# Performance work log

Measured on AMD Instinct MI355X. Metric: run time of the kernel, lower is better.

## Reference

```python
import jax, jax.numpy as jnp
import numpy as np

MODES = 2
N = 6000
KNN = 15
NODES = 512
LC = 3  # number of hidden layers
SCALE = 0.05


def _gen_coo(n, knn):
    # One (row, col) pair per CK_inputs entry: node i couples to 2*(knn+1)
    # neighbors i-knn .. i+knn+1, clipped to valid range. Duplicates at the
    # boundaries are summed on scatter (matches torch sparse coalesce()).
    offsets = np.arange(-knn, knn + 2)            # 2*(knn+1) offsets
    rows = np.repeat(np.arange(n), 2 * (knn + 1))
    cols = np.clip((np.arange(n)[:, None] + offsets[None, :]).reshape(-1), 0, n - 1)
    return rows.astype(np.int32), cols.astype(np.int32)


def setup_inputs() -> dict:
    key = jax.random.key(0)
    k0, k1, k2, k3 = jax.random.split(key, 4)
    CK_inputs = jax.random.normal(k0, (N, 2 * (KNN + 1), 3), dtype=jnp.float32)
    W_in = (jax.random.normal(k1, (3, NODES), dtype=jnp.float32) * SCALE)
    b_in = jnp.zeros((NODES,), dtype=jnp.float32)
    Wh = (jax.random.normal(k2, (LC, NODES, NODES), dtype=jnp.float32) * SCALE)
    bh = jnp.zeros((LC, NODES), dtype=jnp.float32)
    W_out = (jax.random.normal(k3, (NODES, MODES ** 2), dtype=jnp.float32) * SCALE)
    b_out = jnp.zeros((MODES ** 2,), dtype=jnp.float32)
    rows_np, cols_np = _gen_coo(N, KNN)
    return {
        "CK_inputs": CK_inputs,
        "W_in": W_in, "b_in": b_in,
        "Wh": Wh, "bh": bh,
        "W_out": W_out, "b_out": b_out,
        "rows": jnp.asarray(rows_np), "cols": jnp.asarray(cols_np),
    }


def reference(CK_inputs, W_in, b_in, Wh, bh, W_out, b_out, rows, cols):
    n = CK_inputs.shape[0]
    modes = int(np.sqrt(b_out.shape[0]))
    # MLP over all E = N*2*(Knn+1) couplings: [E,3] -> [E, modes^2]
    x = CK_inputs.reshape(-1, 3)
    h = jax.nn.relu(x @ W_in + b_in)
    for l in range(Wh.shape[0]):  # small fixed layer count
        h = jax.nn.relu(h @ Wh[l] + bh[l])
    vals = (h @ W_out + b_out).reshape(-1, modes, modes)  # [E, mi, mj]
    # Fused scatter-add: original builds modes^2 sparse COO tensors with
    # indices (r*modes+mi, c*modes+mj), sums, coalesces, densifies. That is
    # exactly dense[r, mi, c, mj] += vals[e, mi, mj].
    dense = jnp.zeros((n, modes, n, modes), dtype=CK_inputs.dtype)
    dense = dense.at[rows, :, cols, :].add(vals)
    return dense.reshape(n * modes, n * modes)
```

## Files before the change

kernel.cpp:

```cpp
#include <hip/hip_runtime.h>

#define NN     6000
#define KNN    15
#define EPB    32
#define HID    512
#define NLAYER 3
#define OUTDIM 12000
#define MB     96
#define NTH    512
#define NKT    16
#define NG     (NLAYER * NKT)

typedef _Float16 half8  __attribute__((ext_vector_type(8)));
typedef _Float16 half4v __attribute__((ext_vector_type(4)));
typedef float    floatx4 __attribute__((ext_vector_type(4)));

__global__ void prep_weights(const float* __restrict__ Wh, _Float16* __restrict__ Wt)
{
    const int blk = blockIdx.x;
    const int ln  = threadIdx.x;
    const int nt  = blk & 31;
    const int kt  = (blk >> 5) & 15;
    const int l   = blk >> 9;
    const int lc  = ln & 15, lg = ln >> 4;
    const float* src = Wh + (size_t)l * HID * HID
                          + (size_t)(kt * 32 + lg * 8) * HID + nt * 16 + lc;
    half8 v;
#pragma unroll
    for (int j = 0; j < 8; ++j) v[j] = (_Float16)src[(size_t)j * HID];
    *(half8*)(Wt + (size_t)blk * 512 + ln * 8) = v;
}

__global__ __launch_bounds__(NTH, 1)
void mlp_mfma_kernel(const float* __restrict__ CK,
                     const float* __restrict__ W_in,
                     const float* __restrict__ b_in,
                     const float* __restrict__ bh,
                     const float* __restrict__ W_out,
                     const float* __restrict__ b_out,
                     const _Float16* __restrict__ Wt,
                     float4* __restrict__ vals)
{
    extern __shared__ float4 smem4[];
    _Float16* Ah  = (_Float16*)smem4;
    _Float16* Bst = (_Float16*)((char*)smem4 + 98304);
    float*    xs  = (float*)((char*)smem4 + 98304);

    const int t  = threadIdx.x;
    const int w  = t >> 6;
    const int ln = t & 63;
    const int lc = ln & 15;
    const int lg = ln >> 4;
    const int kbase = lg * 8;
    const int swzA  = (lc & 7) << 3;

    if (t < MB * 3) xs[t] = CK[(size_t)blockIdx.x * (MB * 3) + t];
    __syncthreads();

    {
        const int j0 = t;
        const float wi0 = W_in[j0], wi1 = W_in[HID + j0], wi2 = W_in[2 * HID + j0];
        const float bi  = b_in[j0];
#pragma unroll 8
        for (int r = 0; r < MB; ++r) {
            float a = fmaf(xs[r * 3 + 2], wi2,
                      fmaf(xs[r * 3 + 1], wi1,
                      fmaf(xs[r * 3 + 0], wi0, bi)));
            Ah[r * HID + (j0 ^ ((r & 7) << 3))] = (_Float16)fmaxf(a, 0.f);
        }
    }
    __syncthreads();

    half8 rgA[4], rgB[4];
    {
        const half8* s0 = (const half8*)Wt;
        half8 r0[4];
#pragma unroll
        for (int i = 0; i < 4; ++i) r0[i] = s0[i * 512 + t];
        const half8* s1 = (const half8*)Wt + 2048;
#pragma unroll
        for (int i = 0; i < 4; ++i) rgA[i] = s1[i * 512 + t];
        half8* dst = (half8*)Bst;
#pragma unroll
        for (int i = 0; i < 4; ++i) dst[i * 512 + t] = r0[i];
    }
    __syncthreads();

#define KSTEP(G, RCUR, RNXT) do {                                              \
        if ((G) + 2 < NG) {                                                    \
            const half8* src_ = (const half8*)Wt + (size_t)((G) + 2) * 2048;   \
            _Pragma("unroll")                                                  \
            for (int i_ = 0; i_ < 4; ++i_) RNXT[i_] = src_[i_ * 512 + t];      \
        }                                                                      \
        {                                                                      \
            const _Float16* Bcur_ = Bst + (size_t)((G) & 1) * 16384;           \
            half8 b_[4], a_[6];                                                \
            _Pragma("unroll")                                                  \
            for (int nf_ = 0; nf_ < 4; ++nf_)                                  \
                b_[nf_] = *(const half8*)&Bcur_[(w * 4 + nf_) * 512 + ln * 8]; \
            const int kb_ = ((G) & 15) * 32 + kbase;                           \
            _Pragma("unroll")                                                  \
            for (int mf_ = 0; mf_ < 6; ++mf_)                                  \
                a_[mf_] = *(const half8*)&Ah[(mf_ * 16 + lc) * HID + (kb_ ^ swzA)]; \
            __builtin_amdgcn_s_setprio(1);                                     \
            _Pragma("unroll")                                                  \
            for (int mf_ = 0; mf_ < 6; ++mf_)                                  \
                _Pragma("unroll")                                              \
                for (int nf_ = 0; nf_ < 4; ++nf_)                              \
                    acc[mf_][nf_] = __builtin_amdgcn_mfma_f32_16x16x32_f16(    \
                        b_[nf_], a_[mf_], acc[mf_][nf_], 0, 0, 0);             \
            __builtin_amdgcn_s_setprio(0);                                     \
        }                                                                      \
        if ((G) + 1 < NG) {                                                    \
            half8* dst_ = (half8*)Bst + (size_t)(((G) + 1) & 1) * 2048;        \
            _Pragma("unroll")                                                  \
            for (int i_ = 0; i_ < 4; ++i_) dst_[i_ * 512 + t] = RCUR[i_];      \
        }                                                                      \
        __syncthreads();                                                       \
    } while (0)

    for (int layer = 0; layer < NLAYER; ++layer) {
        const float* __restrict__ bias = bh + layer * HID;

        floatx4 acc[6][4];
#pragma unroll
        for (int nf = 0; nf < 4; ++nf) {
            const floatx4 bv = *(const floatx4*)&bias[w * 64 + nf * 16 + lg * 4];
#pragma unroll
            for (int mf = 0; mf < 6; ++mf) acc[mf][nf] = bv;
        }

        for (int kt2 = 0; kt2 < NKT; kt2 += 2) {
            const int g = layer * NKT + kt2;
            KSTEP(g,     rgA, rgB);
            KSTEP(g + 1, rgB, rgA);
        }

#pragma unroll
        for (int mf = 0; mf < 6; ++mf) {
            const int r = mf * 16 + lc;
#pragma unroll
            for (int nf = 0; nf < 4; ++nf) {
                const int n0 = w * 64 + nf * 16 + lg * 4;
                half4v h4;
#pragma unroll
                for (int j = 0; j < 4; ++j)
                    h4[j] = (_Float16)fmaxf(acc[mf][nf][j], 0.f);
                *(half4v*)&Ah[r * HID + (n0 ^ swzA)] = h4;
            }
        }
        __syncthreads();
    }

    {
        const int s = t & 7;
        const float4 bo = *(const float4*)b_out;
#pragma unroll
        for (int pass = 0; pass < 2; ++pass) {
            const int rr = pass * 64 + (t >> 3);
            if (rr < MB) {
                const int swzr = (rr & 7) << 3;
                float p0 = 0.f, p1 = 0.f, p2 = 0.f, p3 = 0.f;
                for (int i = 0; i < HID / 8; ++i) {
                    const int k = s + i * 8;
                    const float hv = (float)Ah[rr * HID + (k ^ swzr)];
                    const floatx4 wv = *(const floatx4*)&W_out[k * 4];
                    p0 = fmaf(hv, wv[0], p0);
                    p1 = fmaf(hv, wv[1], p1);
                    p2 = fmaf(hv, wv[2], p2);
                    p3 = fmaf(hv, wv[3], p3);
                }
#pragma unroll
                for (int m = 1; m < 8; m <<= 1) {
                    p0 += __shfl_xor(p0, m, 64);
                    p1 += __shfl_xor(p1, m, 64);
                    p2 += __shfl_xor(p2, m, 64);
                    p3 += __shfl_xor(p3, m, 64);
                }
                if (s == 0)
                    vals[(size_t)blockIdx.x * MB + rr] =
                        make_float4(p0 + bo.x, p1 + bo.y, p2 + bo.z, p3 + bo.w);
            }
        }
    }
}

__global__ __launch_bounds__(256, 8)
void write_out(const float4* __restrict__ vals, float* __restrict__ out)
{
    const int n = blockIdx.x;
    const int t = threadIdx.x;
    __shared__ float4 v[EPB];
    __shared__ float  band[2][2 * EPB];

    if (t < EPB) v[t] = vals[(size_t)n * EPB + t];
    const int cmin  = (n - KNN < 0) ? 0 : n - KNN;
    const int cmax  = (n + KNN + 1 > NN - 1) ? NN - 1 : n + KNN + 1;
    const int width = cmax - cmin + 1;
    __syncthreads();

    if (t < width) {
        const int c = cmin + t;
        int e_lo, e_hi;
        if (c == 0)           { e_lo = 0;                  e_hi = KNN - n; }
        else if (c == NN - 1) { e_lo = (NN - 1) - n + KNN; e_hi = EPB - 1; }
        else                  { e_lo = e_hi = c - n + KNN; }
        float s0 = 0.f, s1 = 0.f, s2 = 0.f, s3 = 0.f;
        for (int e = e_lo; e <= e_hi; ++e) {
            const float4 pv = v[e];
            s0 += pv.x; s1 += pv.y; s2 += pv.z; s3 += pv.w;
        }
        band[0][2 * t] = s0; band[0][2 * t + 1] = s1;
        band[1][2 * t] = s2; band[1][2 * t + 1] = s3;
    }
    __syncthreads();

    const int j0 = 2 * cmin;
    const int w2 = 2 * width;
#pragma unroll
    for (int mi = 0; mi < 2; ++mi) {
        float* rowp = out + (size_t)(2 * n + mi) * OUTDIM;
        for (int q = t; q < OUTDIM / 4; q += 256) {
            const int j = 4 * q;
            floatx4 o;
            o[0] = ((unsigned)(j + 0 - j0) < (unsigned)w2) ? band[mi][j + 0 - j0] : 0.f;
            o[1] = ((unsigned)(j + 1 - j0) < (unsigned)w2) ? band[mi][j + 1 - j0] : 0.f;
            o[2] = ((unsigned)(j + 2 - j0) < (unsigned)w2) ? band[mi][j + 2 - j0] : 0.f;
            o[3] = ((unsigned)(j + 3 - j0) < (unsigned)w2) ? band[mi][j + 3 - j0] : 0.f;
            __builtin_nontemporal_store(o, (floatx4*)(rowp + j));
        }
    }
}

extern "C" void kernel_launch(void* const* d_in, const int* in_sizes, int n_in,
                              void* d_out, int out_size, void* d_ws, size_t ws_size,
                              hipStream_t stream) {
    const float* CK    = (const float*)d_in[0];
    const float* W_in  = (const float*)d_in[1];
    const float* b_in  = (const float*)d_in[2];
    const float* Wh    = (const float*)d_in[3];
    const float* bh    = (const float*)d_in[4];
    const float* W_out = (const float*)d_in[5];
    const float* b_out = (const float*)d_in[6];
    float* out = (float*)d_out;

    _Float16* Wt   = (_Float16*)d_ws;
    float4*   vals = (float4*)((char*)d_ws + (size_t)3 * HID * HID * sizeof(_Float16));

    (void)ws_size;
    hipFuncSetAttribute((const void*)mlp_mfma_kernel,
                        hipFuncAttributeMaxDynamicSharedMemorySize, 163840);

    prep_weights<<<NLAYER * 16 * 32, 64, 0, stream>>>(Wh, Wt);
    mlp_mfma_kernel<<<NN / 3, NTH, 163840, stream>>>(CK, W_in, b_in, bh, W_out, b_out, Wt, vals);
    write_out<<<NN, 256, 0, stream>>>(vals, out);
}
```

Before: 471.2 us.

## Load MLP weight fragments straight from global into registers, drop LDS staging

Each wave now reads its own B-fragment half8 chunks of the hidden-layer weights directly from global memory into double-buffered registers, instead of cooperatively staging whole k-tiles through LDS. This removes the per-k-step LDS writes, LDS reads and the __syncthreads after every k-step, keeping only one barrier per layer. It also cuts dynamic LDS from 160KB to 96KB. The cost is more scattered global/L2 traffic per wave and reliance on cache bandwidth for weights shared by all blocks.

```diff
diff --git a/kernel.cpp b/kernel.cpp
--- a/kernel.cpp
+++ b/kernel.cpp
@@ -42,9 +42,8 @@
                      float4* __restrict__ vals)
 {
     extern __shared__ float4 smem4[];
-    _Float16* Ah  = (_Float16*)smem4;
-    _Float16* Bst = (_Float16*)((char*)smem4 + 98304);
-    float*    xs  = (float*)((char*)smem4 + 98304);
+    _Float16* Ah = (_Float16*)smem4;
+    __shared__ float xs[MB * 3];
 
     const int t  = threadIdx.x;
     const int w  = t >> 6;
@@ -53,6 +52,14 @@
     const int lg = ln >> 4;
     const int kbase = lg * 8;
     const int swzA  = (lc & 7) << 3;
+
+    const half8* __restrict__ Wt8 = (const half8*)Wt + (size_t)(w * 4) * 64 + ln;
+
+    half8 bA[4], bB[4];
+#pragma unroll
+    for (int nf = 0; nf < 4; ++nf) bA[nf] = Wt8[(size_t)0 * 2048 + nf * 64];
+#pragma unroll
+    for (int nf = 0; nf < 4; ++nf) bB[nf] = Wt8[(size_t)1 * 2048 + nf * 64];
 
     if (t < MB * 3) xs[t] = CK[(size_t)blockIdx.x * (MB * 3) + t];
     __syncthreads();
@@ -71,52 +78,25 @@
     }
     __syncthreads();
 
-    half8 rgA[4], rgB[4];
-    {
-        const half8* s0 = (const half8*)Wt;
-        half8 r0[4];
-#pragma unroll
-        for (int i = 0; i < 4; ++i) r0[i] = s0[i * 512 + t];
-        const half8* s1 = (const half8*)Wt + 2048;
-#pragma unroll
-        for (int i = 0; i < 4; ++i) rgA[i] = s1[i * 512 + t];
-        half8* dst = (half8*)Bst;
-#pragma unroll
-        for (int i = 0; i < 4; ++i) dst[i * 512 + t] = r0[i];
-    }
-    __syncthreads();
-
-#define KSTEP(G, RCUR, RNXT) do {                                              \
-        if ((G) + 2 < NG) {                                                    \
-            const half8* src_ = (const half8*)Wt + (size_t)((G) + 2) * 2048;   \
-            _Pragma("unroll")                                                  \
-            for (int i_ = 0; i_ < 4; ++i_) RNXT[i_] = src_[i_ * 512 + t];      \
-        }                                                                      \
-        {                                                                      \
-            const _Float16* Bcur_ = Bst + (size_t)((G) & 1) * 16384;           \
-            half8 b_[4], a_[6];                                                \
+#define KSTEP(G, RCUR) do {                                                    \
+        half8 a_[6];                                                           \
+        const int kb_ = ((G) & 15) * 32 + kbase;                               \
+        _Pragma("unroll")                                                      \
+        for (int mf_ = 0; mf_ < 6; ++mf_)                                      \
+            a_[mf_] = *(const half8*)&Ah[(mf_ * 16 + lc) * HID + (kb_ ^ swzA)];\
+        __builtin_amdgcn_s_setprio(1);                                         \
+        _Pragma("unroll")                                                      \
+        for (int mf_ = 0; mf_ < 6; ++mf_)                                      \
             _Pragma("unroll")                                                  \
             for (int nf_ = 0; nf_ < 4; ++nf_)                                  \
-                b_[nf_] = *(const half8*)&Bcur_[(w * 4 + nf_) * 512 + ln * 8]; \
-            const int kb_ = ((G) & 15) * 32 + kbase;                           \
+                acc[mf_][nf_] = __builtin_amdgcn_mfma_f32_16x16x32_f16(        \
+                    RCUR[nf_], a_[mf_], acc[mf_][nf_], 0, 0, 0);               \
+        __builtin_amdgcn_s_setprio(0);                                         \
+        if ((G) + 2 < NG) {                                                    \
             _Pragma("unroll")                                                  \
-            for (int mf_ = 0; mf_ < 6; ++mf_)                                  \
-                a_[mf_] = *(const half8*)&Ah[(mf_ * 16 + lc) * HID + (kb_ ^ swzA)]; \
-            __builtin_amdgcn_s_setprio(1);                                     \
-            _Pragma("unroll")                                                  \
-            for (int mf_ = 0; mf_ < 6; ++mf_)                                  \
-                _Pragma("unroll")                                              \
-                for (int nf_ = 0; nf_ < 4; ++nf_)                              \
-                    acc[mf_][nf_] = __builtin_amdgcn_mfma_f32_16x16x32_f16(    \
-                        b_[nf_], a_[mf_], acc[mf_][nf_], 0, 0, 0);             \
-            __builtin_amdgcn_s_setprio(0);                                     \
+            for (int nf_ = 0; nf_ < 4; ++nf_)                                  \
+                RCUR[nf_] = Wt8[(size_t)((G) + 2) * 2048 + nf_ * 64];          \
         }                                                                      \
-        if ((G) + 1 < NG) {                                                    \
-            half8* dst_ = (half8*)Bst + (size_t)(((G) + 1) & 1) * 2048;        \
-            _Pragma("unroll")                                                  \
-            for (int i_ = 0; i_ < 4; ++i_) dst_[i_ * 512 + t] = RCUR[i_];      \
-        }                                                                      \
-        __syncthreads();                                                       \
     } while (0)
 
     for (int layer = 0; layer < NLAYER; ++layer) {
@@ -130,12 +110,14 @@
             for (int mf = 0; mf < 6; ++mf) acc[mf][nf] = bv;
         }
 
+#pragma unroll
         for (int kt2 = 0; kt2 < NKT; kt2 += 2) {
             const int g = layer * NKT + kt2;
-            KSTEP(g,     rgA, rgB);
-            KSTEP(g + 1, rgB, rgA);
-        }
-
+            KSTEP(g,     bA);
+            KSTEP(g + 1, bB);
+        }
+
+        __syncthreads();
 #pragma unroll
         for (int mf = 0; mf < 6; ++mf) {
             const int r = mf * 16 + lc;
@@ -249,9 +231,9 @@
 
     (void)ws_size;
     hipFuncSetAttribute((const void*)mlp_mfma_kernel,
-                        hipFuncAttributeMaxDynamicSharedMemorySize, 163840);
+                        hipFuncAttributeMaxDynamicSharedMemorySize, 98304);
 
     prep_weights<<<NLAYER * 16 * 32, 64, 0, stream>>>(Wh, Wt);
-    mlp_mfma_kernel<<<NN / 3, NTH, 163840, stream>>>(CK, W_in, b_in, bh, W_out, b_out, Wt, vals);
+    mlp_mfma_kernel<<<NN / 3, NTH, 98304, stream>>>(CK, W_in, b_in, bh, W_out, b_out, Wt, vals);
     write_out<<<NN, 256, 0, stream>>>(vals, out);
 }
```

Result: faster. 412.8 us (-12.4%).
